# Optimization experiments

Hardware: AMD Instinct MI355X
Metric: run time of the kernel (lower is better)

## Reference

```python
import jax, jax.numpy as jnp
import numpy as np

N = 4096
C_IN = 256
C_OUT = 256
HEADS = 4
C_HEAD = C_OUT // HEADS
ALPHA = 0.2
NEG_FILL = -9e15


def setup_inputs() -> dict:
    key = jax.random.key(0)
    k1, k2, k3, k4 = jax.random.split(key, 4)
    node_feats = jax.random.normal(k1, (N, C_IN), dtype=jnp.float32)
    adj_matrix = jax.random.randint(k2, (1, N, N), 0, 2, dtype=jnp.int32)
    # xavier_uniform with gain=1.414
    lim_w = 1.414 * np.sqrt(6.0 / (C_IN + C_OUT))
    W = jax.random.uniform(k3, (C_OUT, C_IN), minval=-lim_w, maxval=lim_w, dtype=jnp.float32)
    b = jnp.zeros((C_OUT,), dtype=jnp.float32)
    lim_a = 1.414 * np.sqrt(6.0 / (HEADS + 2 * C_HEAD))
    a = jax.random.uniform(k4, (HEADS, 2 * C_HEAD), minval=-lim_a, maxval=lim_a, dtype=jnp.float32)
    return {"node_feats": node_feats, "adj_matrix": adj_matrix, "W": W, "b": b, "a": a}


def reference(node_feats, adj_matrix, W, b, a):
    # node_feats: [N, c_in] -> batch of 1, as in the torch 2D path
    h = (node_feats @ W.T + b).reshape(1, N, HEADS, C_HEAD)  # [1,N,H,c]
    a_src, a_dst = a[:, :C_HEAD], a[:, C_HEAD:]
    # attn logit for edge (i, j) = leakyrelu(a . [h_i, h_j])
    e_src = jnp.einsum('bnhc,hc->bnh', h, a_src)  # contribution of row node i
    e_dst = jnp.einsum('bnhc,hc->bnh', h, a_dst)  # contribution of col node j
    logits = jax.nn.leaky_relu(e_src[:, :, None, :] + e_dst[:, None, :, :], ALPHA)  # [1,N,N,H]
    mask = (adj_matrix == 1)[..., None]  # [1,N,N,1]
    attn = jnp.where(mask, logits, jnp.float32(NEG_FILL))
    probs = jax.nn.softmax(attn, axis=2)  # softmax over neighbors j
    out = jnp.einsum('bijh,bjhc->bihc', probs, h)  # [1,N,H,c]
    return out.reshape(1, N, HEADS * C_HEAD)  # concat heads
```

## Files before the change

kernel.cpp:

```cpp
#include <hip/hip_runtime.h>
#include <hip/hip_bf16.h>


#define NN 4096
#define LOG2E 1.4426950408889634f

typedef float f32x4 __attribute__((ext_vector_type(4)));
typedef int i32x4 __attribute__((ext_vector_type(4)));
typedef unsigned int u32x2 __attribute__((ext_vector_type(2)));
typedef unsigned int u32x4 __attribute__((ext_vector_type(4)));
typedef unsigned short u16x4 __attribute__((ext_vector_type(4)));
typedef unsigned short u16x8 __attribute__((ext_vector_type(8)));
typedef __bf16 bf16x8 __attribute__((ext_vector_type(8)));

__device__ __forceinline__ unsigned short f2bf_rne(float f) {
    unsigned int u = __builtin_bit_cast(unsigned int, f);
    u += 0x7fffu + ((u >> 16) & 1u);
    return (unsigned short)(u >> 16);
}

__device__ __forceinline__ bf16x8 ld_cvt8(const float* __restrict__ p) {
    f32x4 x = *(const f32x4*)p;
    f32x4 y = *(const f32x4*)(p + 4);
    u16x8 u;
    u[0] = f2bf_rne(x[0]); u[1] = f2bf_rne(x[1]); u[2] = f2bf_rne(x[2]); u[3] = f2bf_rne(x[3]);
    u[4] = f2bf_rne(y[0]); u[5] = f2bf_rne(y[1]); u[6] = f2bf_rne(y[2]); u[7] = f2bf_rne(y[3]);
    return __builtin_bit_cast(bf16x8, u);
}

__global__ __launch_bounds__(256) void k01_fused(const int* __restrict__ adj,
                                                 unsigned int* __restrict__ mb,
                                                 const float* __restrict__ X,
                                                 const float* __restrict__ W,
                                                 const float* __restrict__ bias,
                                                 const float* __restrict__ a,
                                                 unsigned short* __restrict__ hB,
                                                 float* __restrict__ esrc,
                                                 float* __restrict__ edst) {
    if (blockIdx.x < 2048) {
        const int od = blockIdx.x * 256 + threadIdx.x;
        const int i  = od >> 7;
        const int r  = od & 127;
        const int q  = r >> 5;
        const int kg = (r >> 3) & 3;
        const int t0 = (r & 7) * 4;
        const int* src = adj + i * 4096 + q * 1024 + kg * 8;
        unsigned int d = 0;
#pragma unroll
        for (int b = 0; b < 4; ++b) {
            i32x4 v0 = *(const i32x4*)(src + (t0 + b) * 32);
            i32x4 v1 = *(const i32x4*)(src + (t0 + b) * 32 + 4);
#pragma unroll
            for (int e = 0; e < 4; ++e) {
                d |= (unsigned int)(v0[e] & 1) << (b * 8 + e);
                d |= (unsigned int)(v1[e] & 1) << (b * 8 + 4 + e);
            }
        }
        mb[od] = d;
        return;
    }

    const int lane = threadIdx.x & 63;
    const int hh   = threadIdx.x >> 6;
    const int row  = lane & 15;
    const int kg   = lane >> 4;
    const int rowbase = (blockIdx.x - 2048) * 16;

    f32x4 acc[4];
#pragma unroll
    for (int n = 0; n < 4; ++n) acc[n] = (f32x4)0.f;

#pragma unroll
    for (int kk = 0; kk < 8; ++kk) {
        const int kb = kk * 32 + kg * 8;
        bf16x8 a0 = ld_cvt8(X + (rowbase + row) * 256 + kb);
#pragma unroll
        for (int n = 0; n < 4; ++n) {
            bf16x8 bb = ld_cvt8(W + (hh * 64 + n * 16 + row) * 256 + kb);
            acc[n] = __builtin_amdgcn_mfma_f32_16x16x32_bf16(a0, bb, acc[n], 0, 0, 0);
        }
    }

    const int t   = rowbase >> 5;
    const int lp  = (((rowbase >> 4) & 1) * 2 + (kg >> 1)) * 16 + row;
    const int eoff = (kg & 1) * 4;
    unsigned short* hbb = hB + (hh * 128 + t) * 2048 + lp * 8 + eoff;

    float eS0 = 0.f, eS1 = 0.f, eS2 = 0.f, eS3 = 0.f;
    float eT0 = 0.f, eT1 = 0.f, eT2 = 0.f, eT3 = 0.f;
#pragma unroll
    for (int n = 0; n < 4; ++n) {
        const int col = hh * 64 + n * 16 + row;
        const float bv = bias[col];
        f32x4 hv;
        hv[0] = acc[n][0] + bv; hv[1] = acc[n][1] + bv;
        hv[2] = acc[n][2] + bv; hv[3] = acc[n][3] + bv;
        u16x4 us;
        us[0] = f2bf_rne(hv[0]); us[1] = f2bf_rne(hv[1]);
        us[2] = f2bf_rne(hv[2]); us[3] = f2bf_rne(hv[3]);
        *(u16x4*)(hbb + n * 512) = us;
        const float as_ = a[hh * 128 + n * 16 + row];
        const float ad_ = a[hh * 128 + 64 + n * 16 + row];
        eS0 += hv[0] * as_; eS1 += hv[1] * as_; eS2 += hv[2] * as_; eS3 += hv[3] * as_;
        eT0 += hv[0] * ad_; eT1 += hv[1] * ad_; eT2 += hv[2] * ad_; eT3 += hv[3] * ad_;
    }
#pragma unroll
    for (int d = 1; d < 16; d <<= 1) {
        eS0 += __shfl_xor(eS0, d); eS1 += __shfl_xor(eS1, d);
        eS2 += __shfl_xor(eS2, d); eS3 += __shfl_xor(eS3, d);
        eT0 += __shfl_xor(eT0, d); eT1 += __shfl_xor(eT1, d);
        eT2 += __shfl_xor(eT2, d); eT3 += __shfl_xor(eT3, d);
    }
    if (row == 0) {
        const int rb = hh * NN + rowbase + kg * 4;
        esrc[rb + 0] = eS0 * LOG2E; esrc[rb + 1] = eS1 * LOG2E;
        esrc[rb + 2] = eS2 * LOG2E; esrc[rb + 3] = eS3 * LOG2E;
        edst[rb + 0] = eT0 * LOG2E; edst[rb + 1] = eT1 * LOG2E;
        edst[rb + 2] = eT2 * LOG2E; edst[rb + 3] = eT3 * LOG2E;
    }
}

#define K3_MKP(AF, ES, MW, TI) {                                                  \
    f32x4 s0v = E0 + (f32x4)(ES);                                                 \
    f32x4 s1v = E1 + (f32x4)(ES);                                                 \
    s0v = __builtin_elementwise_max(s0v, s0v * 0.2f);                             \
    s1v = __builtin_elementwise_max(s1v, s1v * 0.2f);                             \
    bf16x8 afv;                                                                   \
    afv[0] = (__bf16)__builtin_exp2f(s0v[0]);                                     \
    afv[1] = (__bf16)__builtin_exp2f(s0v[1]);                                     \
    afv[2] = (__bf16)__builtin_exp2f(s0v[2]);                                     \
    afv[3] = (__bf16)__builtin_exp2f(s0v[3]);                                     \
    afv[4] = (__bf16)__builtin_exp2f(s1v[0]);                                     \
    afv[5] = (__bf16)__builtin_exp2f(s1v[1]);                                     \
    afv[6] = (__bf16)__builtin_exp2f(s1v[2]);                                     \
    afv[7] = (__bf16)__builtin_exp2f(s1v[3]);                                     \
    u32x4 aw = __builtin_bit_cast(u32x4, afv);                                    \
    const u32x2 mk0 = mlut[((MW) >> ((TI) * 8)) & 15u];                           \
    const u32x2 mk1 = mlut[((MW) >> ((TI) * 8 + 4)) & 15u];                       \
    aw[0] &= mk0[0]; aw[1] &= mk0[1];                                             \
    aw[2] &= mk1[0]; aw[3] &= mk1[1];                                             \
    AF = __builtin_bit_cast(bf16x8, aw);                                          \
}

__global__ __launch_bounds__(512, 4) void k3_flash(const unsigned int* __restrict__ mb32,
                                                   const unsigned short* __restrict__ hB,
                                                   const float* __restrict__ esrc,
                                                   const float* __restrict__ edst,
                                                   float* __restrict__ out) {
    __shared__ float lacc[8][16][64];
    __shared__ float lls[8][16];
    __shared__ u32x2 mlut[16];

    const int lane = threadIdx.x & 63;
    const int q  = threadIdx.x >> 6;
    const int hh = blockIdx.x & 3;
    const int ib = blockIdx.x >> 2;
    const int i0 = ib * 32;
    const int row = lane & 15;
    const int kg  = lane >> 4;

    if (threadIdx.x < 16) {
        const unsigned n = threadIdx.x;
        u32x2 m;
        m[0] = ((n & 1u) ? 0xFFFFu : 0u) | ((n & 2u) ? 0xFFFF0000u : 0u);
        m[1] = ((n & 4u) ? 0xFFFFu : 0u) | ((n & 8u) ? 0xFFFF0000u : 0u);
        mlut[n] = m;
    }
    __syncthreads();

    const float es0 = esrc[hh * NN + i0 + row];
    const float es1 = esrc[hh * NN + i0 + 16 + row];
    const unsigned int* m0p = mb32 + (i0 + row) * 128 + (q >> 1) * 32 + kg * 8 + (q & 1) * 4;
    const unsigned int* m1p = m0p + 16 * 128;
    const float* eD = edst + hh * NN + q * 512 + kg * 8;
    const unsigned short* hBp = hB + ((hh * 128 + q * 16) * 256 + lane) * 8;

    u16x8 ou;
    const unsigned short ov = (row == 0) ? (unsigned short)0x3F80 : (unsigned short)0;
#pragma unroll
    for (int e = 0; e < 8; ++e) ou[e] = ov;
    const bf16x8 bOnes = __builtin_bit_cast(bf16x8, ou);

    f32x4 aA0 = (f32x4)0.f, aA1 = (f32x4)0.f, aA2 = (f32x4)0.f,
          aA3 = (f32x4)0.f, aA4 = (f32x4)0.f;
    f32x4 aB0 = (f32x4)0.f, aB1 = (f32x4)0.f, aB2 = (f32x4)0.f,
          aB3 = (f32x4)0.f, aB4 = (f32x4)0.f;

    for (int td = 0; td < 4; ++td) {
        const unsigned int M0 = m0p[td];
        const unsigned int M1 = m1p[td];
        const float* eDt = eD + td * 128;
        const unsigned short* hBt = hBp + td * 8192;
#pragma unroll
        for (int ti = 0; ti < 4; ++ti) {
            const f32x4 E0 = *(const f32x4*)(eDt + ti * 32);
            const f32x4 E1 = *(const f32x4*)(eDt + ti * 32 + 4);
            const u16x8 B0 = *(const u16x8*)(hBt + ti * 2048);
            const u16x8 B1 = *(const u16x8*)(hBt + ti * 2048 + 512);
            const u16x8 B2 = *(const u16x8*)(hBt + ti * 2048 + 1024);
            const u16x8 B3 = *(const u16x8*)(hBt + ti * 2048 + 1536);
            bf16x8 af0, af1;
            K3_MKP(af0, es0, M0, ti)
            K3_MKP(af1, es1, M1, ti)
            aA0 = __builtin_amdgcn_mfma_f32_16x16x32_bf16(af0, __builtin_bit_cast(bf16x8, B0), aA0, 0, 0, 0);
            aA1 = __builtin_amdgcn_mfma_f32_16x16x32_bf16(af0, __builtin_bit_cast(bf16x8, B1), aA1, 0, 0, 0);
            aA2 = __builtin_amdgcn_mfma_f32_16x16x32_bf16(af0, __builtin_bit_cast(bf16x8, B2), aA2, 0, 0, 0);
            aA3 = __builtin_amdgcn_mfma_f32_16x16x32_bf16(af0, __builtin_bit_cast(bf16x8, B3), aA3, 0, 0, 0);
            aA4 = __builtin_amdgcn_mfma_f32_16x16x32_bf16(af0, bOnes, aA4, 0, 0, 0);
            aB0 = __builtin_amdgcn_mfma_f32_16x16x32_bf16(af1, __builtin_bit_cast(bf16x8, B0), aB0, 0, 0, 0);
            aB1 = __builtin_amdgcn_mfma_f32_16x16x32_bf16(af1, __builtin_bit_cast(bf16x8, B1), aB1, 0, 0, 0);
            aB2 = __builtin_amdgcn_mfma_f32_16x16x32_bf16(af1, __builtin_bit_cast(bf16x8, B2), aB2, 0, 0, 0);
            aB3 = __builtin_amdgcn_mfma_f32_16x16x32_bf16(af1, __builtin_bit_cast(bf16x8, B3), aB3, 0, 0, 0);
            aB4 = __builtin_amdgcn_mfma_f32_16x16x32_bf16(af1, bOnes, aB4, 0, 0, 0);
        }
    }

#pragma unroll
    for (int n = 0; n < 4; ++n) {
        f32x4 an = (n == 0) ? aA0 : (n == 1) ? aA1 : (n == 2) ? aA2 : aA3;
#pragma unroll
        for (int r = 0; r < 4; ++r)
            lacc[q][kg * 4 + r][n * 16 + row] = an[r];
    }
    if (row == 0) {
#pragma unroll
        for (int r = 0; r < 4; ++r) lls[q][kg * 4 + r] = aA4[r];
    }
    __syncthreads();
    if (threadIdx.x < 256) {
        const int idx = threadIdx.x * 4;
        const int r2 = idx >> 6;
        const int c  = idx & 63;
        f32x4 v = (f32x4)0.f;
        float l = 0.f;
#pragma unroll
        for (int q2 = 0; q2 < 8; ++q2) {
            v += *(const f32x4*)&lacc[q2][r2][c];
            l += lls[q2][r2];
        }
        const float inv = 1.f / l;
        f32x4 o;
        o[0] = v[0] * inv; o[1] = v[1] * inv; o[2] = v[2] * inv; o[3] = v[3] * inv;
        *(f32x4*)(out + (i0 + r2) * 256 + hh * 64 + c) = o;
    }
    __syncthreads();

#pragma unroll
    for (int n = 0; n < 4; ++n) {
        f32x4 an = (n == 0) ? aB0 : (n == 1) ? aB1 : (n == 2) ? aB2 : aB3;
#pragma unroll
        for (int r = 0; r < 4; ++r)
            lacc[q][kg * 4 + r][n * 16 + row] = an[r];
    }
    if (row == 0) {
#pragma unroll
        for (int r = 0; r < 4; ++r) lls[q][kg * 4 + r] = aB4[r];
    }
    __syncthreads();
    if (threadIdx.x < 256) {
        const int idx = threadIdx.x * 4;
        const int r2 = idx >> 6;
        const int c  = idx & 63;
        f32x4 v = (f32x4)0.f;
        float l = 0.f;
#pragma unroll
        for (int q2 = 0; q2 < 8; ++q2) {
            v += *(const f32x4*)&lacc[q2][r2][c];
            l += lls[q2][r2];
        }
        const float inv = 1.f / l;
        f32x4 o;
        o[0] = v[0] * inv; o[1] = v[1] * inv; o[2] = v[2] * inv; o[3] = v[3] * inv;
        *(f32x4*)(out + (i0 + 16 + r2) * 256 + hh * 64 + c) = o;
    }
}

extern "C" void kernel_launch(void* const* d_in, const int* in_sizes, int n_in,
                              void* d_out, int out_size, void* d_ws, size_t ws_size,
                              hipStream_t stream) {
    const float* X    = (const float*)d_in[0];
    const int*   adj  = (const int*)d_in[1];
    const float* W    = (const float*)d_in[2];
    const float* bias = (const float*)d_in[3];
    const float* a    = (const float*)d_in[4];
    float* out = (float*)d_out;

    char* ws = (char*)d_ws;
    unsigned int*   mb   = (unsigned int*)(ws);
    unsigned short* hB   = (unsigned short*)(ws + (2 << 20));
    float*          esrc = (float*)(ws + (4 << 20));
    float*          edst = (float*)(ws + (4 << 20) + (64 << 10));

    k01_fused<<<2304, 256, 0, stream>>>(adj, mb, X, W, bias, a, hB, esrc, edst);
    k3_flash<<<512, 512, 0, stream>>>(mb, hB, esrc, edst, out);
}
```

Measured before the change: 64.84 us.

## Split adjacency packing into its own kernel with a simple contiguous bit layout

```diff
diff --git a/kernel.cpp b/kernel.cpp
--- a/kernel.cpp
+++ b/kernel.cpp
@@ -28,43 +28,34 @@
     return __builtin_bit_cast(bf16x8, u);
 }
 
-__global__ __launch_bounds__(256) void k01_fused(const int* __restrict__ adj,
-                                                 unsigned int* __restrict__ mb,
-                                                 const float* __restrict__ X,
-                                                 const float* __restrict__ W,
-                                                 const float* __restrict__ bias,
-                                                 const float* __restrict__ a,
-                                                 unsigned short* __restrict__ hB,
-                                                 float* __restrict__ esrc,
-                                                 float* __restrict__ edst) {
-    if (blockIdx.x < 2048) {
-        const int od = blockIdx.x * 256 + threadIdx.x;
-        const int i  = od >> 7;
-        const int r  = od & 127;
-        const int q  = r >> 5;
-        const int kg = (r >> 3) & 3;
-        const int t0 = (r & 7) * 4;
-        const int* src = adj + i * 4096 + q * 1024 + kg * 8;
-        unsigned int d = 0;
-#pragma unroll
-        for (int b = 0; b < 4; ++b) {
-            i32x4 v0 = *(const i32x4*)(src + (t0 + b) * 32);
-            i32x4 v1 = *(const i32x4*)(src + (t0 + b) * 32 + 4);
-#pragma unroll
-            for (int e = 0; e < 4; ++e) {
-                d |= (unsigned int)(v0[e] & 1) << (b * 8 + e);
-                d |= (unsigned int)(v1[e] & 1) << (b * 8 + 4 + e);
-            }
-        }
-        mb[od] = d;
-        return;
-    }
-
+__global__ __launch_bounds__(256) void k0_pack(const int* __restrict__ adj,
+                                               unsigned int* __restrict__ mw) {
+    const int wi = blockIdx.x * 256 + threadIdx.x;
+    const int* src = adj + wi * 32;
+    unsigned int w = 0;
+#pragma unroll
+    for (int c = 0; c < 8; ++c) {
+        const i32x4 v = *(const i32x4*)(src + c * 4);
+        w |= (unsigned)(v[0] & 1) << (c * 4 + 0);
+        w |= (unsigned)(v[1] & 1) << (c * 4 + 1);
+        w |= (unsigned)(v[2] & 1) << (c * 4 + 2);
+        w |= (unsigned)(v[3] & 1) << (c * 4 + 3);
+    }
+    mw[wi] = w;
+}
+
+__global__ __launch_bounds__(256) void k1_fused(const float* __restrict__ X,
+                                                const float* __restrict__ W,
+                                                const float* __restrict__ bias,
+                                                const float* __restrict__ a,
+                                                unsigned short* __restrict__ hB,
+                                                float* __restrict__ esrc,
+                                                float* __restrict__ edst) {
     const int lane = threadIdx.x & 63;
     const int hh   = threadIdx.x >> 6;
     const int row  = lane & 15;
     const int kg   = lane >> 4;
-    const int rowbase = (blockIdx.x - 2048) * 16;
+    const int rowbase = blockIdx.x * 16;
 
     f32x4 acc[4];
 #pragma unroll
@@ -120,7 +111,7 @@
     }
 }
 
-#define K3_MKP(AF, ES, MW, TI) {                                                  \
+#define K3_MKP(AF, ES, MW) {                                                      \
     f32x4 s0v = E0 + (f32x4)(ES);                                                 \
     f32x4 s1v = E1 + (f32x4)(ES);                                                 \
     s0v = __builtin_elementwise_max(s0v, s0v * 0.2f);                             \
@@ -135,14 +126,14 @@
     afv[6] = (__bf16)__builtin_exp2f(s1v[2]);                                     \
     afv[7] = (__bf16)__builtin_exp2f(s1v[3]);                                     \
     u32x4 aw = __builtin_bit_cast(u32x4, afv);                                    \
-    const u32x2 mk0 = mlut[((MW) >> ((TI) * 8)) & 15u];                           \
-    const u32x2 mk1 = mlut[((MW) >> ((TI) * 8 + 4)) & 15u];                       \
+    const u32x2 mk0 = mlut[((MW) >> kg8) & 15u];                                  \
+    const u32x2 mk1 = mlut[(((MW) >> kg8) >> 4) & 15u];                           \
     aw[0] &= mk0[0]; aw[1] &= mk0[1];                                             \
     aw[2] &= mk1[0]; aw[3] &= mk1[1];                                             \
     AF = __builtin_bit_cast(bf16x8, aw);                                          \
 }
 
-__global__ __launch_bounds__(512, 4) void k3_flash(const unsigned int* __restrict__ mb32,
+__global__ __launch_bounds__(512, 4) void k3_flash(const unsigned int* __restrict__ mw32,
                                                    const unsigned short* __restrict__ hB,
                                                    const float* __restrict__ esrc,
                                                    const float* __restrict__ edst,
@@ -158,6 +149,7 @@
     const int i0 = ib * 32;
     const int row = lane & 15;
     const int kg  = lane >> 4;
+    const int kg8 = kg * 8;
 
     if (threadIdx.x < 16) {
         const unsigned n = threadIdx.x;
@@ -170,8 +162,7 @@
 
     const float es0 = esrc[hh * NN + i0 + row];
     const float es1 = esrc[hh * NN + i0 + 16 + row];
-    const unsigned int* m0p = mb32 + (i0 + row) * 128 + (q >> 1) * 32 + kg * 8 + (q & 1) * 4;
-    const unsigned int* m1p = m0p + 16 * 128;
+    const unsigned int* mwp = mw32 + (i0 + row) * 128 + q * 16;
     const float* eD = edst + hh * NN + q * 512 + kg * 8;
     const unsigned short* hBp = hB + ((hh * 128 + q * 16) * 256 + lane) * 8;
 
@@ -187,8 +178,8 @@
           aB3 = (f32x4)0.f, aB4 = (f32x4)0.f;
 
     for (int td = 0; td < 4; ++td) {
-        const unsigned int M0 = m0p[td];
-        const unsigned int M1 = m1p[td];
+        const u32x4 M0 = *(const u32x4*)(mwp + td * 4);
+        const u32x4 M1 = *(const u32x4*)(mwp + 16 * 128 + td * 4);
         const float* eDt = eD + td * 128;
         const unsigned short* hBt = hBp + td * 8192;
 #pragma unroll
@@ -200,8 +191,8 @@
             const u16x8 B2 = *(const u16x8*)(hBt + ti * 2048 + 1024);
             const u16x8 B3 = *(const u16x8*)(hBt + ti * 2048 + 1536);
             bf16x8 af0, af1;
-            K3_MKP(af0, es0, M0, ti)
-            K3_MKP(af1, es1, M1, ti)
+            K3_MKP(af0, es0, M0[ti])
+            K3_MKP(af1, es1, M1[ti])
             aA0 = __builtin_amdgcn_mfma_f32_16x16x32_bf16(af0, __builtin_bit_cast(bf16x8, B0), aA0, 0, 0, 0);
             aA1 = __builtin_amdgcn_mfma_f32_16x16x32_bf16(af0, __builtin_bit_cast(bf16x8, B1), aA1, 0, 0, 0);
             aA2 = __builtin_amdgcn_mfma_f32_16x16x32_bf16(af0, __builtin_bit_cast(bf16x8, B2), aA2, 0, 0, 0);
@@ -286,11 +277,12 @@
     float* out = (float*)d_out;
 
     char* ws = (char*)d_ws;
-    unsigned int*   mb   = (unsigned int*)(ws);
+    unsigned int*   mw   = (unsigned int*)(ws);
     unsigned short* hB   = (unsigned short*)(ws + (2 << 20));
     float*          esrc = (float*)(ws + (4 << 20));
     float*          edst = (float*)(ws + (4 << 20) + (64 << 10));
 
-    k01_fused<<<2304, 256, 0, stream>>>(adj, mb, X, W, bias, a, hB, esrc, edst);
-    k3_flash<<<512, 512, 0, stream>>>(mb, hB, esrc, edst, out);
-}
+    k0_pack<<<2048, 256, 0, stream>>>(adj, mw);
+    k1_fused<<<256, 256, 0, stream>>>(X, W, bias, a, hB, esrc, edst);
+    k3_flash<<<512, 512, 0, stream>>>(mw, hB, esrc, edst, out);
+}
```

New measurement: 56.44 us. -13.0%, faster.
